# Kernel tuning notes

Measured on AMD Instinct MI355X. Metric: run time of the kernel, lower is better.

## Reference

```python
import jax, jax.numpy as jnp
import numpy as np
from functools import partial

NUM_HEADS = 12
NUM_CLUSTERS = 98
LN_EPS = 1e-5
INF = 1e10


def _ln(x, g, b):
    m = x.mean(-1, keepdims=True)
    v = ((x - m) ** 2).mean(-1, keepdims=True)
    return (x - m) / jnp.sqrt(v + LN_EPS) * g + b


def _agglom(dist, num_clusters):
    # dist: [T,T] precomputed distances; average-linkage agglomerative clustering.
    T = dist.shape[0]
    D = dist.at[jnp.arange(T), jnp.arange(T)].set(INF)
    sizes = jnp.ones((T,), dist.dtype)
    labels = jnp.arange(T)
    active = jnp.ones((T,), bool)

    def step(_, state):
        D, sizes, labels, active = state
        Dm = jnp.where(active[:, None] & active[None, :], D, INF)
        idx = jnp.argmin(Dm)
        i0, j0 = idx // T, idx % T
        i = jnp.minimum(i0, j0)
        j = jnp.maximum(i0, j0)
        ni, nj = sizes[i], sizes[j]
        # Lance-Williams update for average linkage
        newd = (ni * D[i] + nj * D[j]) / (ni + nj)
        D = D.at[i, :].set(newd).at[:, i].set(newd)
        D = D.at[i, i].set(INF)
        D = D.at[j, :].set(INF).at[:, j].set(INF)
        sizes = sizes.at[i].set(ni + nj)
        labels = jnp.where(labels == j, i, labels)
        active = active.at[j].set(False)
        return (D, sizes, labels, active)

    D, sizes, labels, active = jax.lax.fori_loop(0, T - num_clusters, step, (D, sizes, labels, active))
    rank = jnp.cumsum(active.astype(jnp.int32)) - 1  # compact active cluster ids to 0..K-1
    return rank[labels]


def reference(x, attn_size, n1_g, n1_b, w_qkv, w_proj, b_proj, n2_g, n2_b, w_fc1, b_fc1, w_fc2, b_fc2):
    B, N, C = x.shape
    H = NUM_HEADS
    hd = C // H
    # --- Attention_ToMe ---
    h = _ln(x, n1_g, n1_b)
    qkv = (h @ w_qkv).reshape(B, N, 3, H, hd).transpose(2, 0, 3, 1, 4)
    q, k, v = qkv[0], qkv[1], qkv[2]
    metric = k.mean(axis=1)  # [B,N,hd]
    attn = jnp.einsum('bhqd,bhkd->bhqk', q, k) * (hd ** -0.5)
    attn = attn + jnp.log(attn_size)[:, None, None, :, 0]  # size bias (log 1 = 0 first block)
    attn = jax.nn.softmax(attn, axis=-1)
    xa = jnp.einsum('bhqk,bhkd->bqhd', attn, v).reshape(B, N, C)
    x = x + xa @ w_proj + b_proj
    # --- agglomerative clustering (no_grad in original) ---
    m = jax.lax.stop_gradient(metric)
    m = m / jnp.linalg.norm(m, axis=-1, keepdims=True)
    dist = 1.0 - jnp.einsum('bnd,bmd->bnm', m, m)[:, 1:, 1:]  # drop cls token
    labels = jax.vmap(partial(_agglom, num_clusters=NUM_CLUSTERS))(dist)  # [B,N-1]
    labels = jnp.concatenate([jnp.zeros((B, 1), labels.dtype), labels + 1], axis=1)  # cls -> cluster 0
    # --- weighted-average merge (scatter_reduce sum expressed as onehot matmul) ---
    Kt = NUM_CLUSTERS + 1
    onehot = (labels[:, :, None] == jnp.arange(Kt)[None, None, :]).astype(x.dtype)  # [B,N,Kt]
    xs = jnp.einsum('bnk,bnc->bkc', onehot, x * attn_size)
    size_new = jnp.einsum('bnk,bnc->bkc', onehot, attn_size)
    x = xs / size_new
    # --- MLP ---
    h = _ln(x, n2_g, n2_b)
    h = jax.nn.gelu(h @ w_fc1 + b_fc1, approximate=False)
    x = x + h @ w_fc2 + b_fc2
    return x, size_new, labels


def setup_inputs() -> dict:
    key = jax.random.key(0)
    ks = jax.random.split(key, 6)
    B, N, C = 64, 197, 768
    Hf = 4 * C
    s = lambda d: 1.0 / np.sqrt(d)
    return {
        'x': jax.random.normal(ks[0], (B, N, C), jnp.float32),
        'attn_size': jnp.ones((B, N, 1), jnp.float32),
        'n1_g': jnp.ones((C,), jnp.float32),
        'n1_b': jnp.zeros((C,), jnp.float32),
        'w_qkv': jax.random.normal(ks[1], (C, 3 * C), jnp.float32) * s(C),
        'w_proj': jax.random.normal(ks[2], (C, C), jnp.float32) * s(C),
        'b_proj': jnp.zeros((C,), jnp.float32),
        'n2_g': jnp.ones((C,), jnp.float32),
        'n2_b': jnp.zeros((C,), jnp.float32),
        'w_fc1': jax.random.normal(ks[3], (C, Hf), jnp.float32) * s(C),
        'b_fc1': jnp.zeros((Hf,), jnp.float32),
        'w_fc2': jax.random.normal(ks[4], (Hf, C), jnp.float32) * s(Hf),
        'b_fc2': jnp.zeros((C,), jnp.float32),
    }
```

## Files before the change

### kernel.cpp

```cpp
#include <hip/hip_runtime.h>
#include <hip/hip_bf16.h>
#include <math.h>

#define INF_ 1e10f
#define LGKM0() asm volatile("s_waitcnt lgkmcnt(0)" ::: "memory")

static constexpr int B_  = 64;
static constexpr int N_  = 197;
static constexpr int C_  = 768;
static constexpr int H_  = 12;
static constexpr int T_  = 196;
static constexpr int KC_ = 98;
static constexpr int KT_ = 99;
static constexpr int HF_ = 3072;

typedef __attribute__((ext_vector_type(8))) short short8v;
typedef __attribute__((ext_vector_type(4))) float f32x4;
typedef __attribute__((ext_vector_type(4))) int int4v;

__device__ __forceinline__ float wave_sum(float v){
#pragma unroll
  for(int o=32;o;o>>=1) v += __shfl_down(v,o);
  return v;
}

__device__ __forceinline__ ushort f2bf(float v){
  __hip_bfloat16 t = __float2bfloat16(v);
  return *reinterpret_cast<const ushort*>(&t);
}

__device__ __forceinline__ unsigned long long packkey(float v, int r, int a){
  unsigned int bb = __float_as_uint(v);
  bb ^= (bb & 0x80000000u) ? 0xFFFFFFFFu : 0x80000000u;
  return ((unsigned long long)bb<<32) | (unsigned)(r<<8) | (unsigned)a;
}
__device__ __forceinline__ float unpackval(unsigned long long key){
  unsigned u = (unsigned)(key>>32);
  u = (u & 0x80000000u) ? (u ^ 0x80000000u) : ~u;
  return __uint_as_float(u);
}

__global__ __launch_bounds__(256) void ln_kernel(const float* __restrict__ in,
    const float* __restrict__ g, const float* __restrict__ bb,
    float* __restrict__ outf, __hip_bfloat16* __restrict__ outb){
  int row = blockIdx.x;
  const float* xr = in + (size_t)row*C_;
  int tid = threadIdx.x;
  float v0=xr[tid], v1=xr[tid+256], v2=xr[tid+512];
  __shared__ float sred[4];
  __shared__ float smean, svar;
  float s = wave_sum(v0+v1+v2);
  int w=tid>>6, l=tid&63;
  if(l==0) sred[w]=s;
  __syncthreads();
  if(tid==0) smean = (sred[0]+sred[1]+sred[2]+sred[3])/(float)C_;
  __syncthreads();
  float m = smean;
  float d0=v0-m, d1=v1-m, d2=v2-m;
  float q = wave_sum(d0*d0+d1*d1+d2*d2);
  if(l==0) sred[w]=q;
  __syncthreads();
  if(tid==0) svar = (sred[0]+sred[1]+sred[2]+sred[3])/(float)C_;
  __syncthreads();
  float sq = sqrtf(svar + 1e-5f);
  float y0 = d0/sq*g[tid]     + bb[tid];
  float y1 = d1/sq*g[tid+256] + bb[tid+256];
  float y2 = d2/sq*g[tid+512] + bb[tid+512];
  if(outf){
    float* orow = outf + (size_t)row*C_;
    orow[tid]=y0; orow[tid+256]=y1; orow[tid+512]=y2;
  }
  if(outb){
    __hip_bfloat16* orow = outb + (size_t)row*C_;
    orow[tid]=__float2bfloat16(y0); orow[tid+256]=__float2bfloat16(y1); orow[tid+512]=__float2bfloat16(y2);
  }
}

__global__ __launch_bounds__(256) void wmean_kernel(const float* __restrict__ w,
    float* __restrict__ Wm){
  int t = blockIdx.x*256 + threadIdx.x;
  if(t >= C_*64) return;
  int c = t>>6, d = t&63;
  const float* p = w + (size_t)c*(3*C_) + C_ + d;
  float s=0.f;
#pragma unroll
  for(int h=0;h<H_;h++) s += p[h*64];
  Wm[t] = s*(1.0f/12.0f);
}

__global__ __launch_bounds__(256) void transpose_bf16(const float* __restrict__ w,
    __hip_bfloat16* __restrict__ wt, int K, int N){
  __shared__ float tile[32][33];
  int n0 = blockIdx.x*32, k0 = blockIdx.y*32;
  int tx = threadIdx.x&31, ty = threadIdx.x>>5;
  for(int r=ty;r<32;r+=8) tile[r][tx] = w[(size_t)(k0+r)*N + n0+tx];
  __syncthreads();
  for(int r=ty;r<32;r+=8) wt[(size_t)(n0+r)*K + k0+tx] = __float2bfloat16(tile[tx][r]);
}

template<int EPI>
__global__ __launch_bounds__(256) void gemm_bf16(const ushort* __restrict__ A,
    const ushort* __restrict__ Bt, const float* __restrict__ bias,
    const float* __restrict__ res, void* __restrict__ Cout,
    int M, int N, int K){
  constexpr int BM=128, BN=128, BK=32;
  __shared__ ushort As[BM][40];
  __shared__ ushort Bs[BN][40];
  int tid = threadIdx.x;
  int bm = blockIdx.y*BM, bn = blockIdx.x*BN;
  int w = tid>>6, l = tid&63;
  int wm = (w>>1)*64, wn = (w&1)*64;
  int lr = l&15, lc = l>>4;
  f32x4 acc[4][4] = {};
  for(int k0=0;k0<K;k0+=BK){
#pragma unroll
    for(int s=0;s<2;s++){
      int cid = tid + s*256;
      int r = cid>>2, ch = cid&3;
      int4v va = {0,0,0,0};
      if(bm+r < M) va = *reinterpret_cast<const int4v*>(A + (size_t)(bm+r)*K + k0 + ch*8);
      *reinterpret_cast<int4v*>(&As[r][ch*8]) = va;
      int4v vb = *reinterpret_cast<const int4v*>(Bt + (size_t)(bn+r)*K + k0 + ch*8);
      *reinterpret_cast<int4v*>(&Bs[r][ch*8]) = vb;
    }
    __syncthreads();
    short8v af[4], bfr[4];
#pragma unroll
    for(int f=0; f<4; f++){
      af[f]  = *reinterpret_cast<const short8v*>(&As[wm + f*16 + lr][lc*8]);
      bfr[f] = *reinterpret_cast<const short8v*>(&Bs[wn + f*16 + lr][lc*8]);
    }
#pragma unroll
    for(int i=0;i<4;i++)
#pragma unroll
      for(int j=0;j<4;j++)
        acc[i][j] = __builtin_amdgcn_mfma_f32_16x16x32_bf16(af[i], bfr[j], acc[i][j], 0,0,0);
    __syncthreads();
  }
#pragma unroll
  for(int i=0;i<4;i++){
    int rbase = bm + wm + i*16 + lc*4;
#pragma unroll
    for(int j=0;j<4;j++){
      int col = bn + wn + j*16 + lr;
#pragma unroll
      for(int r=0;r<4;r++){
        int row = rbase + r;
        if(row >= M) continue;
        size_t idx = (size_t)row*N + col;
        float v = acc[i][j][r];
        if constexpr(EPI==1 || EPI==3) ((float*)Cout)[idx] = (res[idx] + v) + bias[col];
        if constexpr(EPI==2){
          v += bias[col];
          v = 0.5f*v*(1.0f+erff(v*0.70710678118654752f));
          ((__hip_bfloat16*)Cout)[idx] = __float2bfloat16(v);
        }
        if constexpr(EPI==4) ((__hip_bfloat16*)Cout)[idx] = __float2bfloat16(v);
      }
    }
  }
}

__global__ __launch_bounds__(256) void metric_gemm(const float* __restrict__ h,
    const float* __restrict__ Wm, float* __restrict__ mnorm){
  int row0 = blockIdx.x*16;
  __shared__ float hs[16][C_];
  int tid = threadIdx.x;
  int w = tid>>6, l = tid&63;
  for(int t=tid; t<16*C_; t+=256)
    hs[t/C_][t%C_] = h[(size_t)row0*C_ + t];
  __syncthreads();
  float a0=0.f,a1=0.f,a2=0.f,a3=0.f;
#pragma unroll 4
  for(int c=0;c<C_;c++){
    float wv = Wm[c*64+l];
    a0 = fmaf(hs[w*4+0][c], wv, a0);
    a1 = fmaf(hs[w*4+1][c], wv, a1);
    a2 = fmaf(hs[w*4+2][c], wv, a2);
    a3 = fmaf(hs[w*4+3][c], wv, a3);
  }
  float accs[4] = {a0,a1,a2,a3};
#pragma unroll
  for(int r=0;r<4;r++){
    float acc = accs[r];
    float q = acc*acc;
#pragma unroll
    for(int o=32;o;o>>=1) q += __shfl_xor(q,o);
    float nrm = sqrtf(q);
    int row = row0 + w*4 + r;
    int bb = row / N_, n = row - bb*N_;
    if(n>=1) mnorm[((size_t)bb*T_+(n-1))*64+l] = acc/nrm;
  }
}

__global__ __launch_bounds__(256) void attn_mfma(const ushort* __restrict__ qkv,
    const float* __restrict__ attn_size, __hip_bfloat16* __restrict__ xa){
  int h = blockIdx.x, b = blockIdx.y;
  __shared__ ushort Ks[208][72];
  __shared__ ushort VsT[64][232];
  __shared__ ushort Ps[4][16][232];
  __shared__ float lsz[208];
  int tid = threadIdx.x;
  int w = tid>>6, l = tid&63;
  int lr = l&15, lc = l>>4;
  const size_t QROW = 3*C_;
  for(int t=tid; t<208*64; t+=256){
    int n=t>>6, d=t&63;
    ushort v = 0;
    if(n<197) v = qkv[((size_t)(b*N_+n))*QROW + C_ + h*64 + d];
    Ks[n][d] = v;
  }
  for(int t=tid; t<232*64; t+=256){
    int n=t>>6, d=t&63;
    ushort v = 0;
    if(n<197) v = qkv[((size_t)(b*N_+n))*QROW + 2*C_ + h*64 + d];
    VsT[d][n] = v;
  }
  for(int t=tid;t<208;t+=256) lsz[t] = (t<197)? logf(attn_size[b*N_+t]) : 0.f;
  for(int c=l; c<16*24; c+=64){ int rr=c/24, cc=208+(c%24); Ps[w][rr][cc]=0; }
  __syncthreads();

  for(int qt=w; qt<13; qt+=4){
    int qrow = min(qt*16 + lr, 196);
    const ushort* qp = qkv + ((size_t)(b*N_+qrow))*QROW + h*64;
    short8v aq0 = *reinterpret_cast<const short8v*>(qp + lc*8);
    short8v aq1 = *reinterpret_cast<const short8v*>(qp + 32 + lc*8);
    float sc[13][4];
#pragma unroll
    for(int t=0;t<13;t++){
      short8v b0 = *reinterpret_cast<const short8v*>(&Ks[t*16+lr][lc*8]);
      short8v b1 = *reinterpret_cast<const short8v*>(&Ks[t*16+lr][32+lc*8]);
      f32x4 a = {0.f,0.f,0.f,0.f};
      a = __builtin_amdgcn_mfma_f32_16x16x32_bf16(aq0, b0, a, 0,0,0);
      a = __builtin_amdgcn_mfma_f32_16x16x32_bf16(aq1, b1, a, 0,0,0);
      float ls = lsz[t*16+lr];
      bool mask = (t==12) && (lr>=5);
#pragma unroll
      for(int r=0;r<4;r++) sc[t][r] = mask ? -1e30f : (a[r]*0.125f + ls);
    }
    float rsum[4];
#pragma unroll
    for(int r=0;r<4;r++){
      float m=-1e30f;
#pragma unroll
      for(int t=0;t<13;t++) m = fmaxf(m, sc[t][r]);
#pragma unroll
      for(int o=1;o<16;o<<=1) m = fmaxf(m, __shfl_xor(m,o));
      float s=0.f;
#pragma unroll
      for(int t=0;t<13;t++){ float p=expf(sc[t][r]-m); sc[t][r]=p; s+=p; }
#pragma unroll
      for(int o=1;o<16;o<<=1) s += __shfl_xor(s,o);
      rsum[r]=s;
    }
#pragma unroll
    for(int t=0;t<13;t++)
#pragma unroll
      for(int r=0;r<4;r++)
        Ps[w][lc*4+r][t*16+lr] = f2bf(sc[t][r]);
    LGKM0();
    short8v ap[7];
#pragma unroll
    for(int ks=0;ks<7;ks++) ap[ks] = *reinterpret_cast<const short8v*>(&Ps[w][lr][ks*32 + lc*8]);
#pragma unroll
    for(int f=0; f<4; f++){
      f32x4 o = {0.f,0.f,0.f,0.f};
#pragma unroll
      for(int ks=0;ks<7;ks++){
        short8v bv = *reinterpret_cast<const short8v*>(&VsT[f*16+lr][ks*32 + lc*8]);
        o = __builtin_amdgcn_mfma_f32_16x16x32_bf16(ap[ks], bv, o, 0,0,0);
      }
#pragma unroll
      for(int r=0;r<4;r++){
        int q = qt*16 + lc*4 + r;
        if(q<197) xa[((size_t)(b*N_+q))*C_ + h*64 + f*16 + lr] = __float2bfloat16(o[r]/rsum[r]);
      }
    }
  }
}

__global__ __launch_bounds__(256) void cluster_kernel(const float* __restrict__ mnorm,
    int* __restrict__ labs_ws, float* __restrict__ labs_out){
  int b = blockIdx.x;
  __shared__ unsigned long long rowkey[T_];
  __shared__ unsigned long long gkey[2][4];
  __shared__ unsigned long long scratch[4];
  __shared__ float D[T_][T_+1];
  __shared__ float sizes[T_];
  __shared__ int   labels[T_];
  __shared__ int   active[T_];
  __shared__ int   rlist[T_];
  __shared__ int   rcnt;
  int tid = threadIdx.x;
  int w = tid>>6, l = tid&63;
  const float* mb = mnorm + (size_t)b*T_*64;

  for(int t=tid;t<T_*T_;t+=256){
    int r=t/T_, c=t%T_;
    float dot=0.0f;
    for(int d=0;d<64;d++) dot += mb[r*64+d]*mb[c*64+d];
    D[r][c] = (r==c) ? INF_ : (1.0f - dot);
  }
  for(int t=tid;t<T_;t+=256){ sizes[t]=1.0f; labels[t]=t; active[t]=1; }
  if(tid<8) gkey[tid>>2][tid&3] = ~0ULL;
  __syncthreads();
  if(tid<T_){
    float bvv=INF_; int ba=0;
    for(int c=0;c<T_;c++){ float v=D[tid][c]; if(v<bvv){ bvv=v; ba=c; } }
    rowkey[tid] = packkey(bvv, tid, ba);
  }
  __syncthreads();

  for(int it=0; it<T_-KC_; it++){
    int p = it&1;
    unsigned long long key = (tid<T_) ? rowkey[tid] : ~0ULL;
    atomicMin(&gkey[p][w], key);
    if(tid==0) rcnt = 0;
    __syncthreads();
    unsigned long long g0=gkey[p][0], g1=gkey[p][1];
    unsigned long long g2=gkey[p][2], g3=gkey[p][3];
    unsigned long long ga = g0<g1?g0:g1, gb2 = g2<g3?g2:g3;
    unsigned long long g  = ga<gb2?ga:gb2;
    int i = (int)((g>>8)&0xFF);
    int j = (int)(g&0xFF);
    float ni = sizes[i], nj = sizes[j];
    int k=tid;
    if(k<T_){
      float di=D[i][k], dj=D[j][k];
      unsigned long long oldkey = rowkey[k];
      float oldrm = unpackval(oldkey);
      int oldarg = (int)(oldkey & 0xFF);
      bool kact = (k!=i) && (k!=j) && (active[k]!=0);
      float nd = kact ? (ni*di + nj*dj) / (ni+nj) : INF_;
      D[i][k]=nd; D[k][i]=nd; D[j][k]=INF_; D[k][j]=INF_;
      if(labels[k]==j) labels[k]=i;
      if(k==i){
        int q=atomicAdd(&rcnt,1); rlist[q]=k;
      } else if(k==j){
        rowkey[k] = packkey(INF_, k, 0);
      } else if(kact){
        if(oldarg==i){
          if(nd<=oldrm) rowkey[k] = packkey(nd, k, i);
          else { int q=atomicAdd(&rcnt,1); rlist[q]=k; }
        } else if(oldarg==j){
          if(nd<=oldrm) rowkey[k] = packkey(nd, k, i);
          else { int q=atomicAdd(&rcnt,1); rlist[q]=k; }
        } else {
          if(nd<oldrm || (nd==oldrm && i<oldarg)) rowkey[k] = packkey(nd, k, i);
        }
      }
    }
    if(tid==0){ sizes[i]=ni+nj; active[j]=0; }
    if(l==0) atomicExch(&gkey[p^1][w], ~0ULL);
    __syncthreads();
    int nr = rcnt;
    for(int q=w; q<nr; q+=4){
      int rr = rlist[q];
      if(l==0) atomicExch(&scratch[w], ~0ULL);
      unsigned long long lk = ~0ULL;
      for(int cc=l; cc<T_; cc+=64){
        unsigned long long ck = packkey(D[rr][cc], rr, cc);
        if(ck<lk) lk=ck;
      }
      atomicMin(&scratch[w], lk);
      LGKM0();
      unsigned long long rk = scratch[w];
      if(l==0) rowkey[rr] = rk;
    }
    __syncthreads();
  }

  if(tid==0){
    int c=0;
    for(int t=0;t<T_;t++){ c += active[t]; rlist[t]=c-1; }
    labs_ws[b*N_]=0; labs_out[b*N_]=0.0f;
  }
  __syncthreads();
  for(int t=tid;t<T_;t+=256){
    int lab = rlist[labels[t]] + 1;
    labs_ws[b*N_+1+t] = lab;
    labs_out[b*N_+1+t] = (float)lab;
  }
}

__global__ __launch_bounds__(256) void merge_kernel(const float* __restrict__ x1,
    const float* __restrict__ asz, const int* __restrict__ labs,
    float* __restrict__ x2, float* __restrict__ size_out){
  int chunk = blockIdx.x;
  int b = blockIdx.y;
  __shared__ float acc[KT_][256];
  __shared__ int   lab[N_];
  __shared__ float sz[N_];
  __shared__ float ssum[KT_];
  int tid = threadIdx.x;
  for(int t=tid;t<N_;t+=256){ lab[t]=labs[b*N_+t]; sz[t]=asz[b*N_+t]; }
#pragma unroll
  for(int k=0;k<KT_;k++) acc[k][tid]=0.f;
  __syncthreads();
  if(tid<KT_){
    float s=0.f;
    for(int n=0;n<N_;n++) if(lab[n]==tid) s += sz[n];
    ssum[tid]=s;
  }
  int c = chunk*256 + tid;
  const float* xb = x1 + (size_t)b*N_*C_ + c;
  for(int n=0;n<N_;n++){
    float v = xb[(size_t)n*C_];
    int k = lab[n];
    acc[k][tid] += v * sz[n];
  }
  __syncthreads();
  for(int k=0;k<KT_;k++)
    x2[((size_t)(b*KT_+k))*C_ + c] = acc[k][tid] / ssum[k];
  if(chunk==0 && tid<KT_) size_out[b*KT_+tid] = ssum[tid];
}

extern "C" void kernel_launch(void* const* d_in, const int* in_sizes, int n_in,
                              void* d_out, int out_size, void* d_ws, size_t ws_size,
                              hipStream_t stream){
  const float* x      = (const float*)d_in[0];
  const float* asz    = (const float*)d_in[1];
  const float* n1_g   = (const float*)d_in[2];
  const float* n1_b   = (const float*)d_in[3];
  const float* w_qkv  = (const float*)d_in[4];
  const float* w_proj = (const float*)d_in[5];
  const float* b_proj = (const float*)d_in[6];
  const float* n2_g   = (const float*)d_in[7];
  const float* n2_b   = (const float*)d_in[8];
  const float* w_fc1  = (const float*)d_in[9];
  const float* b_fc1  = (const float*)d_in[10];
  const float* w_fc2  = (const float*)d_in[11];
  const float* b_fc2  = (const float*)d_in[12];

  const size_t ROWS = (size_t)B_*N_;
  const size_t M2   = (size_t)B_*KT_;
  float* ws = (float*)d_ws;

  float* h     = ws;
  float* qkvR  = h + ROWS*C_;
  __hip_bfloat16* qkvb = (__hip_bfloat16*)qkvR;
  float* x2    = qkvR;
  __hip_bfloat16* h2b = (__hip_bfloat16*)(qkvR + M2*C_);
  __hip_bfloat16* h3b = (__hip_bfloat16*)(qkvR + M2*C_ + M2*C_/2);
  __hip_bfloat16* hb  = (__hip_bfloat16*)(qkvR + ROWS*3*C_);
  __hip_bfloat16* xa  = hb;
  float* mnorm = (float*)(hb) + ROWS*C_/2;
  float* Wm    = mnorm + (size_t)B_*T_*64;
  __hip_bfloat16* wqkvT = (__hip_bfloat16*)(Wm + C_*64);
  __hip_bfloat16* wprojT= (__hip_bfloat16*)((float*)wqkvT + (size_t)3*C_*C_/2);
  __hip_bfloat16* wfc1T = (__hip_bfloat16*)((float*)wprojT + (size_t)C_*C_/2);
  __hip_bfloat16* wfc2T = (__hip_bfloat16*)((float*)wfc1T + (size_t)C_*HF_/2);
  int*   labs  = (int*)((float*)wfc2T + (size_t)HF_*C_/2);
  float* x1    = h;

  float* out     = (float*)d_out;
  float* out_sz  = out + M2*C_;
  float* out_lab = out_sz + M2;

  ln_kernel<<<dim3((unsigned)ROWS),256,0,stream>>>(x, n1_g, n1_b, h, hb);
  wmean_kernel<<<dim3(192),256,0,stream>>>(w_qkv, Wm);
  transpose_bf16<<<dim3(72,24),256,0,stream>>>(w_qkv, wqkvT, C_, 3*C_);
  transpose_bf16<<<dim3(24,24),256,0,stream>>>(w_proj, wprojT, C_, C_);
  transpose_bf16<<<dim3(96,24),256,0,stream>>>(w_fc1, wfc1T, C_, HF_);
  transpose_bf16<<<dim3(24,96),256,0,stream>>>(w_fc2, wfc2T, HF_, C_);

  gemm_bf16<4><<<dim3(18,99),256,0,stream>>>((const ushort*)hb, (const ushort*)wqkvT,
      nullptr, nullptr, qkvb, (int)ROWS, 3*C_, C_);
  metric_gemm<<<dim3(788),256,0,stream>>>(h, Wm, mnorm);
  attn_mfma<<<dim3(H_,B_),256,0,stream>>>((const ushort*)qkvb, asz, xa);
  gemm_bf16<1><<<dim3(6,99),256,0,stream>>>((const ushort*)xa, (const ushort*)wprojT,
      b_proj, x, x1, (int)ROWS, C_, C_);

  cluster_kernel<<<dim3(B_),256,0,stream>>>(mnorm, labs, out_lab);
  merge_kernel<<<dim3(3,B_),256,0,stream>>>(x1, asz, labs, x2, out_sz);

  ln_kernel<<<dim3((unsigned)M2),256,0,stream>>>(x2, n2_g, n2_b, nullptr, h2b);
  gemm_bf16<2><<<dim3(24,50),256,0,stream>>>((const ushort*)h2b, (const ushort*)wfc1T,
      b_fc1, nullptr, h3b, (int)M2, HF_, C_);
  gemm_bf16<3><<<dim3(6,50),256,0,stream>>>((const ushort*)h3b, (const ushort*)wfc2T,
      b_fc2, x2, out, (int)M2, C_, HF_);
}
```

Baseline: 1.158 ms.

## Cut clustering loop to one barrier per merge with register state and triple-buffered keys

Restructures the agglomerative clustering loop so each merge step needs a single __syncthreads instead of two. Per-row min keys, sizes, labels and active flags move into registers. The merged row's new min is found by an atomicMin reduction folded into the update. Global-min keys are triple-buffered so resetting the slot for a later step does not race with readers, and dirty rows are rescanned serially by their owning thread instead of cooperatively by a wave. The barrier saving is traded for possible thread divergence on the serial 196-element rescans.

```diff
diff --git a/kernel.cpp b/kernel.cpp
--- a/kernel.cpp
+++ b/kernel.cpp
@@ -282,17 +282,15 @@
 __global__ __launch_bounds__(256) void cluster_kernel(const float* __restrict__ mnorm,
     int* __restrict__ labs_ws, float* __restrict__ labs_out){
   int b = blockIdx.x;
-  __shared__ unsigned long long rowkey[T_];
-  __shared__ unsigned long long gkey[2][4];
-  __shared__ unsigned long long scratch[4];
   __shared__ float D[T_][T_+1];
-  __shared__ float sizes[T_];
-  __shared__ int   labels[T_];
-  __shared__ int   active[T_];
-  __shared__ int   rlist[T_];
-  __shared__ int   rcnt;
-  int tid = threadIdx.x;
-  int w = tid>>6, l = tid&63;
+  __shared__ unsigned long long gkey[3][4];
+  __shared__ unsigned long long rikey[3][4];
+  __shared__ float szl[2][256];
+  __shared__ int labels_s[T_];
+  __shared__ int act_s[T_];
+  __shared__ int rank_s[T_];
+  int tid = threadIdx.x;
+  int w = tid>>6;
   const float* mb = mnorm + (size_t)b*T_*64;
 
   for(int t=tid;t<T_*T_;t+=256){
@@ -301,83 +299,88 @@
     for(int d=0;d<64;d++) dot += mb[r*64+d]*mb[c*64+d];
     D[r][c] = (r==c) ? INF_ : (1.0f - dot);
   }
-  for(int t=tid;t<T_;t+=256){ sizes[t]=1.0f; labels[t]=t; active[t]=1; }
-  if(tid<8) gkey[tid>>2][tid&3] = ~0ULL;
-  __syncthreads();
+  if(tid<12) gkey[tid>>2][tid&3] = ~0ULL;
+  else if(tid<24) rikey[(tid-12)>>2][(tid-12)&3] = ~0ULL;
+  szl[0][tid]=1.0f; szl[1][tid]=1.0f;
+  __syncthreads();
+
+  unsigned long long mykey = ~0ULL;
+  float szk = 1.0f;
+  int labk = tid;
+  int actk = (tid<T_) ? 1 : 0;
   if(tid<T_){
-    float bvv=INF_; int ba=0;
-    for(int c=0;c<T_;c++){ float v=D[tid][c]; if(v<bvv){ bvv=v; ba=c; } }
-    rowkey[tid] = packkey(bvv, tid, ba);
-  }
-  __syncthreads();
-
+    float bv=INF_; int ba=0;
+    for(int c=0;c<T_;c++){ float v=D[tid][c]; if(v<bv){bv=v;ba=c;} }
+    mykey = packkey(bv, tid, ba);
+    atomicMin(&gkey[0][w], mykey);
+  }
+  __syncthreads();
+
+  int iprev = -1;
   for(int it=0; it<T_-KC_; it++){
-    int p = it&1;
-    unsigned long long key = (tid<T_) ? rowkey[tid] : ~0ULL;
-    atomicMin(&gkey[p][w], key);
-    if(tid==0) rcnt = 0;
-    __syncthreads();
-    unsigned long long g0=gkey[p][0], g1=gkey[p][1];
-    unsigned long long g2=gkey[p][2], g3=gkey[p][3];
-    unsigned long long ga = g0<g1?g0:g1, gb2 = g2<g3?g2:g3;
-    unsigned long long g  = ga<gb2?ga:gb2;
+    int A = it%3, Bs = (it+1)%3, Cs = (it+2)%3;
+    int pA = it&1, pB = pA^1;
+    unsigned long long g=~0ULL, rik=~0ULL;
+#pragma unroll
+    for(int s=0;s<4;s++){ unsigned long long v=gkey[A][s]; if(v<g) g=v; }
+#pragma unroll
+    for(int s=0;s<4;s++){ unsigned long long v=rikey[A][s]; if(v<rik) rik=v; }
+    if(tid==iprev) mykey = rik;
+    if(rik<g) g = rik;
     int i = (int)((g>>8)&0xFF);
     int j = (int)(g&0xFF);
-    float ni = sizes[i], nj = sizes[j];
-    int k=tid;
-    if(k<T_){
+    float ni = szl[pA][i], nj = szl[pA][j];
+    if(tid==i) szk = ni+nj;
+    if(tid==j) actk = 0;
+    if(labk==j) labk = i;
+    szl[pB][tid] = szk;
+    if((tid&63)==0){ gkey[Cs][w]=~0ULL; rikey[Cs][w]=~0ULL; }
+    if(tid<T_){
+      int k = tid;
       float di=D[i][k], dj=D[j][k];
-      unsigned long long oldkey = rowkey[k];
-      float oldrm = unpackval(oldkey);
-      int oldarg = (int)(oldkey & 0xFF);
-      bool kact = (k!=i) && (k!=j) && (active[k]!=0);
-      float nd = kact ? (ni*di + nj*dj) / (ni+nj) : INF_;
+      float oldrm = unpackval(mykey);
+      int oldarg = (int)(mykey & 0xFF);
+      bool kact = (k!=i) && (k!=j) && (actk!=0);
+      float nd = kact ? (ni*di + nj*dj)/(ni+nj) : INF_;
       D[i][k]=nd; D[k][i]=nd; D[j][k]=INF_; D[k][j]=INF_;
-      if(labels[k]==j) labels[k]=i;
+      atomicMin(&rikey[Bs][w], packkey(nd, i, k));
       if(k==i){
-        int q=atomicAdd(&rcnt,1); rlist[q]=k;
       } else if(k==j){
-        rowkey[k] = packkey(INF_, k, 0);
+        mykey = packkey(INF_, k, 0);
       } else if(kact){
+        bool dirty=false;
         if(oldarg==i){
-          if(nd<=oldrm) rowkey[k] = packkey(nd, k, i);
-          else { int q=atomicAdd(&rcnt,1); rlist[q]=k; }
+          if(nd<=oldrm) mykey=packkey(nd,k,i); else dirty=true;
         } else if(oldarg==j){
-          if(nd<=oldrm) rowkey[k] = packkey(nd, k, i);
-          else { int q=atomicAdd(&rcnt,1); rlist[q]=k; }
+          if(nd<=oldrm) mykey=packkey(nd,k,i); else dirty=true;
         } else {
-          if(nd<oldrm || (nd==oldrm && i<oldarg)) rowkey[k] = packkey(nd, k, i);
+          if(nd<oldrm || (nd==oldrm && i<oldarg)) mykey=packkey(nd,k,i);
         }
+        if(dirty){
+          float v=INF_; int cb=0;
+          for(int cc=0;cc<T_;cc++){
+            float vv = D[k][cc];
+            if(vv<v){ v=vv; cb=cc; }
+          }
+          mykey = packkey(v,k,cb);
+        }
+        atomicMin(&gkey[Bs][w], mykey);
       }
     }
-    if(tid==0){ sizes[i]=ni+nj; active[j]=0; }
-    if(l==0) atomicExch(&gkey[p^1][w], ~0ULL);
+    iprev = i;
     __syncthreads();
-    int nr = rcnt;
-    for(int q=w; q<nr; q+=4){
-      int rr = rlist[q];
-      if(l==0) atomicExch(&scratch[w], ~0ULL);
-      unsigned long long lk = ~0ULL;
-      for(int cc=l; cc<T_; cc+=64){
-        unsigned long long ck = packkey(D[rr][cc], rr, cc);
-        if(ck<lk) lk=ck;
-      }
-      atomicMin(&scratch[w], lk);
-      LGKM0();
-      unsigned long long rk = scratch[w];
-      if(l==0) rowkey[rr] = rk;
-    }
-    __syncthreads();
-  }
-
+  }
+
+  if(tid<T_){ labels_s[tid]=labk; act_s[tid]=actk; }
+  __syncthreads();
   if(tid==0){
     int c=0;
-    for(int t=0;t<T_;t++){ c += active[t]; rlist[t]=c-1; }
+    for(int t=0;t<T_;t++){ c += act_s[t]; rank_s[t]=c-1; }
     labs_ws[b*N_]=0; labs_out[b*N_]=0.0f;
   }
   __syncthreads();
   for(int t=tid;t<T_;t+=256){
-    int lab = rlist[labels[t]] + 1;
+    int lab = rank_s[labels_s[t]] + 1;
     labs_ws[b*N_+1+t] = lab;
     labs_out[b*N_+1+t] = (float)lab;
   }
```

Result: slower. 1.498 ms (+29.4%).

## Run clustering concurrently with attention in one launch and merge weight-prep kernels

Applied to the files above, without the earlier changes.

Merges the weight-mean and four weight-transpose kernels into a single prep kernel that dispatches on block index. Fuses the serial per-batch clustering kernel with the attention kernel into one launch, with the first 64 blocks doing clustering and the rest doing attention over a shared-memory union. The aim is to hide the long, low-occupancy clustering loop behind the attention work and to cut launch overhead. The union is sized by the larger clustering layout, so attention blocks now reserve more LDS, which may lower their occupancy.

```diff
diff --git a/kernel.cpp b/kernel.cpp
--- a/kernel.cpp
+++ b/kernel.cpp
@@ -76,23 +76,33 @@
   }
 }
 
-__global__ __launch_bounds__(256) void wmean_kernel(const float* __restrict__ w,
-    float* __restrict__ Wm){
-  int t = blockIdx.x*256 + threadIdx.x;
-  if(t >= C_*64) return;
-  int c = t>>6, d = t&63;
-  const float* p = w + (size_t)c*(3*C_) + C_ + d;
-  float s=0.f;
-#pragma unroll
-  for(int h=0;h<H_;h++) s += p[h*64];
-  Wm[t] = s*(1.0f/12.0f);
-}
-
-__global__ __launch_bounds__(256) void transpose_bf16(const float* __restrict__ w,
-    __hip_bfloat16* __restrict__ wt, int K, int N){
+__global__ __launch_bounds__(256) void prep_kernel(const float* __restrict__ w_qkv,
+    const float* __restrict__ w_proj, const float* __restrict__ w_fc1,
+    const float* __restrict__ w_fc2, float* __restrict__ Wm,
+    __hip_bfloat16* __restrict__ wqkvT, __hip_bfloat16* __restrict__ wprojT,
+    __hip_bfloat16* __restrict__ wfc1T, __hip_bfloat16* __restrict__ wfc2T){
+  int bid = blockIdx.x;
+  int tid = threadIdx.x;
+  if(bid < 192){
+    int t = bid*256 + tid;
+    if(t >= C_*64) return;
+    int c = t>>6, d = t&63;
+    const float* p = w_qkv + (size_t)c*(3*C_) + C_ + d;
+    float s=0.f;
+#pragma unroll
+    for(int h=0;h<H_;h++) s += p[h*64];
+    Wm[t] = s*(1.0f/12.0f);
+    return;
+  }
+  bid -= 192;
+  const float* w; __hip_bfloat16* wt; int K, N, nbx;
+  if(bid < 1728){ w=w_qkv; wt=wqkvT; K=C_; N=3*C_; nbx=72; }
+  else if(bid < 1728+576){ bid-=1728; w=w_proj; wt=wprojT; K=C_; N=C_; nbx=24; }
+  else if(bid < 1728+576+2304){ bid-=1728+576; w=w_fc1; wt=wfc1T; K=C_; N=HF_; nbx=96; }
+  else { bid-=1728+576+2304; w=w_fc2; wt=wfc2T; K=HF_; N=C_; nbx=24; }
   __shared__ float tile[32][33];
-  int n0 = blockIdx.x*32, k0 = blockIdx.y*32;
-  int tx = threadIdx.x&31, ty = threadIdx.x>>5;
+  int n0 = (bid%nbx)*32, k0 = (bid/nbx)*32;
+  int tx = tid&31, ty = tid>>5;
   for(int r=ty;r<32;r+=8) tile[r][tx] = w[(size_t)(k0+r)*N + n0+tx];
   __syncthreads();
   for(int r=ty;r<32;r+=8) wt[(size_t)(n0+r)*K + k0+tx] = __float2bfloat16(tile[tx][r]);
@@ -193,13 +203,121 @@
   }
 }
 
-__global__ __launch_bounds__(256) void attn_mfma(const ushort* __restrict__ qkv,
-    const float* __restrict__ attn_size, __hip_bfloat16* __restrict__ xa){
-  int h = blockIdx.x, b = blockIdx.y;
-  __shared__ ushort Ks[208][72];
-  __shared__ ushort VsT[64][232];
-  __shared__ ushort Ps[4][16][232];
-  __shared__ float lsz[208];
+struct ClusterSh {
+  float D[T_][T_+1];
+  unsigned long long rowkey[T_];
+  unsigned long long gkey[2][4];
+  unsigned long long scratch[4];
+  float sizes[T_];
+  int labels[T_];
+  int active[T_];
+  int rlist[T_];
+  int rcnt;
+};
+struct AttnSh {
+  ushort Ks[208][72];
+  ushort VsT[64][232];
+  ushort Ps[4][16][232];
+  float lsz[208];
+};
+union FusedSh { ClusterSh c; AttnSh a; };
+
+__device__ void cluster_body(ClusterSh& S, const float* __restrict__ mnorm,
+    int* __restrict__ labs_ws, float* __restrict__ labs_out, int b){
+  int tid = threadIdx.x;
+  int w = tid>>6, l = tid&63;
+  const float* mb = mnorm + (size_t)b*T_*64;
+
+  for(int t=tid;t<T_*T_;t+=256){
+    int r=t/T_, c=t%T_;
+    float dot=0.0f;
+    for(int d=0;d<64;d++) dot += mb[r*64+d]*mb[c*64+d];
+    S.D[r][c] = (r==c) ? INF_ : (1.0f - dot);
+  }
+  for(int t=tid;t<T_;t+=256){ S.sizes[t]=1.0f; S.labels[t]=t; S.active[t]=1; }
+  if(tid<8) S.gkey[tid>>2][tid&3] = ~0ULL;
+  __syncthreads();
+  if(tid<T_){
+    float bvv=INF_; int ba=0;
+    for(int c=0;c<T_;c++){ float v=S.D[tid][c]; if(v<bvv){ bvv=v; ba=c; } }
+    S.rowkey[tid] = packkey(bvv, tid, ba);
+  }
+  __syncthreads();
+
+  for(int it=0; it<T_-KC_; it++){
+    int p = it&1;
+    unsigned long long key = (tid<T_) ? S.rowkey[tid] : ~0ULL;
+    atomicMin(&S.gkey[p][w], key);
+    if(tid==0) S.rcnt = 0;
+    __syncthreads();
+    unsigned long long g0=S.gkey[p][0], g1=S.gkey[p][1];
+    unsigned long long g2=S.gkey[p][2], g3=S.gkey[p][3];
+    unsigned long long ga = g0<g1?g0:g1, gb2 = g2<g3?g2:g3;
+    unsigned long long g  = ga<gb2?ga:gb2;
+    int i = (int)((g>>8)&0xFF);
+    int j = (int)(g&0xFF);
+    float ni = S.sizes[i], nj = S.sizes[j];
+    int k=tid;
+    if(k<T_){
+      float di=S.D[i][k], dj=S.D[j][k];
+      unsigned long long oldkey = S.rowkey[k];
+      float oldrm = unpackval(oldkey);
+      int oldarg = (int)(oldkey & 0xFF);
+      bool kact = (k!=i) && (k!=j) && (S.active[k]!=0);
+      float nd = kact ? (ni*di + nj*dj) / (ni+nj) : INF_;
+      S.D[i][k]=nd; S.D[k][i]=nd; S.D[j][k]=INF_; S.D[k][j]=INF_;
+      if(S.labels[k]==j) S.labels[k]=i;
+      if(k==i){
+        int q=atomicAdd(&S.rcnt,1); S.rlist[q]=k;
+      } else if(k==j){
+        S.rowkey[k] = packkey(INF_, k, 0);
+      } else if(kact){
+        if(oldarg==i){
+          if(nd<=oldrm) S.rowkey[k] = packkey(nd, k, i);
+          else { int q=atomicAdd(&S.rcnt,1); S.rlist[q]=k; }
+        } else if(oldarg==j){
+          if(nd<=oldrm) S.rowkey[k] = packkey(nd, k, i);
+          else { int q=atomicAdd(&S.rcnt,1); S.rlist[q]=k; }
+        } else {
+          if(nd<oldrm || (nd==oldrm && i<oldarg)) S.rowkey[k] = packkey(nd, k, i);
+        }
+      }
+    }
+    if(tid==0){ S.sizes[i]=ni+nj; S.active[j]=0; }
+    if(l==0) atomicExch(&S.gkey[p^1][w], ~0ULL);
+    __syncthreads();
+    int nr = S.rcnt;
+    for(int q=w; q<nr; q+=4){
+      int rr = S.rlist[q];
+      if(l==0) atomicExch(&S.scratch[w], ~0ULL);
+      unsigned long long lk = ~0ULL;
+      for(int cc=l; cc<T_; cc+=64){
+        unsigned long long ck = packkey(S.D[rr][cc], rr, cc);
+        if(ck<lk) lk=ck;
+      }
+      atomicMin(&S.scratch[w], lk);
+      LGKM0();
+      unsigned long long rk = S.scratch[w];
+      if(l==0) S.rowkey[rr] = rk;
+    }
+    __syncthreads();
+  }
+
+  if(tid==0){
+    int c=0;
+    for(int t=0;t<T_;t++){ c += S.active[t]; S.rlist[t]=c-1; }
+    labs_ws[b*N_]=0; labs_out[b*N_]=0.0f;
+  }
+  __syncthreads();
+  for(int t=tid;t<T_;t+=256){
+    int lab = S.rlist[S.labels[t]] + 1;
+    labs_ws[b*N_+1+t] = lab;
+    labs_out[b*N_+1+t] = (float)lab;
+  }
+}
+
+__device__ void attn_body(AttnSh& S, const ushort* __restrict__ qkv,
+    const float* __restrict__ attn_size, __hip_bfloat16* __restrict__ xa, int h, int b){
   int tid = threadIdx.x;
   int w = tid>>6, l = tid&63;
   int lr = l&15, lc = l>>4;
@@ -208,16 +326,16 @@
     int n=t>>6, d=t&63;
     ushort v = 0;
     if(n<197) v = qkv[((size_t)(b*N_+n))*QROW + C_ + h*64 + d];
-    Ks[n][d] = v;
+    S.Ks[n][d] = v;
   }
   for(int t=tid; t<232*64; t+=256){
     int n=t>>6, d=t&63;
     ushort v = 0;
     if(n<197) v = qkv[((size_t)(b*N_+n))*QROW + 2*C_ + h*64 + d];
-    VsT[d][n] = v;
-  }
-  for(int t=tid;t<208;t+=256) lsz[t] = (t<197)? logf(attn_size[b*N_+t]) : 0.f;
-  for(int c=l; c<16*24; c+=64){ int rr=c/24, cc=208+(c%24); Ps[w][rr][cc]=0; }
+    S.VsT[d][n] = v;
+  }
+  for(int t=tid;t<208;t+=256) S.lsz[t] = (t<197)? logf(attn_size[b*N_+t]) : 0.f;
+  for(int c=l; c<16*24; c+=64){ int rr=c/24, cc=208+(c%24); S.Ps[w][rr][cc]=0; }
   __syncthreads();
 
   for(int qt=w; qt<13; qt+=4){
@@ -228,12 +346,12 @@
     float sc[13][4];
 #pragma unroll
     for(int t=0;t<13;t++){
-      short8v b0 = *reinterpret_cast<const short8v*>(&Ks[t*16+lr][lc*8]);
-      short8v b1 = *reinterpret_cast<const short8v*>(&Ks[t*16+lr][32+lc*8]);
+      short8v b0 = *reinterpret_cast<const short8v*>(&S.Ks[t*16+lr][lc*8]);
+      short8v b1 = *reinterpret_cast<const short8v*>(&S.Ks[t*16+lr][32+lc*8]);
       f32x4 a = {0.f,0.f,0.f,0.f};
       a = __builtin_amdgcn_mfma_f32_16x16x32_bf16(aq0, b0, a, 0,0,0);
       a = __builtin_amdgcn_mfma_f32_16x16x32_bf16(aq1, b1, a, 0,0,0);
-      float ls = lsz[t*16+lr];
+      float ls = S.lsz[t*16+lr];
       bool mask = (t==12) && (lr>=5);
 #pragma unroll
       for(int r=0;r<4;r++) sc[t][r] = mask ? -1e30f : (a[r]*0.125f + ls);
@@ -257,17 +375,17 @@
     for(int t=0;t<13;t++)
 #pragma unroll
       for(int r=0;r<4;r++)
-        Ps[w][lc*4+r][t*16+lr] = f2bf(sc[t][r]);
+        S.Ps[w][lc*4+r][t*16+lr] = f2bf(sc[t][r]);
     LGKM0();
     short8v ap[7];
 #pragma unroll
-    for(int ks=0;ks<7;ks++) ap[ks] = *reinterpret_cast<const short8v*>(&Ps[w][lr][ks*32 + lc*8]);
+    for(int ks=0;ks<7;ks++) ap[ks] = *reinterpret_cast<const short8v*>(&S.Ps[w][lr][ks*32 + lc*8]);
 #pragma unroll
     for(int f=0; f<4; f++){
       f32x4 o = {0.f,0.f,0.f,0.f};
 #pragma unroll
       for(int ks=0;ks<7;ks++){
-        short8v bv = *reinterpret_cast<const short8v*>(&VsT[f*16+lr][ks*32 + lc*8]);
+        short8v bv = *reinterpret_cast<const short8v*>(&S.VsT[f*16+lr][ks*32 + lc*8]);
         o = __builtin_amdgcn_mfma_f32_16x16x32_bf16(ap[ks], bv, o, 0,0,0);
       }
 #pragma unroll
@@ -279,107 +397,17 @@
   }
 }
 
-__global__ __launch_bounds__(256) void cluster_kernel(const float* __restrict__ mnorm,
-    int* __restrict__ labs_ws, float* __restrict__ labs_out){
-  int b = blockIdx.x;
-  __shared__ unsigned long long rowkey[T_];
-  __shared__ unsigned long long gkey[2][4];
-  __shared__ unsigned long long scratch[4];
-  __shared__ float D[T_][T_+1];
-  __shared__ float sizes[T_];
-  __shared__ int   labels[T_];
-  __shared__ int   active[T_];
-  __shared__ int   rlist[T_];
-  __shared__ int   rcnt;
-  int tid = threadIdx.x;
-  int w = tid>>6, l = tid&63;
-  const float* mb = mnorm + (size_t)b*T_*64;
-
-  for(int t=tid;t<T_*T_;t+=256){
-    int r=t/T_, c=t%T_;
-    float dot=0.0f;
-    for(int d=0;d<64;d++) dot += mb[r*64+d]*mb[c*64+d];
-    D[r][c] = (r==c) ? INF_ : (1.0f - dot);
-  }
-  for(int t=tid;t<T_;t+=256){ sizes[t]=1.0f; labels[t]=t; active[t]=1; }
-  if(tid<8) gkey[tid>>2][tid&3] = ~0ULL;
-  __syncthreads();
-  if(tid<T_){
-    float bvv=INF_; int ba=0;
-    for(int c=0;c<T_;c++){ float v=D[tid][c]; if(v<bvv){ bvv=v; ba=c; } }
-    rowkey[tid] = packkey(bvv, tid, ba);
-  }
-  __syncthreads();
-
-  for(int it=0; it<T_-KC_; it++){
-    int p = it&1;
-    unsigned long long key = (tid<T_) ? rowkey[tid] : ~0ULL;
-    atomicMin(&gkey[p][w], key);
-    if(tid==0) rcnt = 0;
-    __syncthreads();
-    unsigned long long g0=gkey[p][0], g1=gkey[p][1];
-    unsigned long long g2=gkey[p][2], g3=gkey[p][3];
-    unsigned long long ga = g0<g1?g0:g1, gb2 = g2<g3?g2:g3;
-    unsigned long long g  = ga<gb2?ga:gb2;
-    int i = (int)((g>>8)&0xFF);
-    int j = (int)(g&0xFF);
-    float ni = sizes[i], nj = sizes[j];
-    int k=tid;
-    if(k<T_){
-      float di=D[i][k], dj=D[j][k];
-      unsigned long long oldkey = rowkey[k];
-      float oldrm = unpackval(oldkey);
-      int oldarg = (int)(oldkey & 0xFF);
-      bool kact = (k!=i) && (k!=j) && (active[k]!=0);
-      float nd = kact ? (ni*di + nj*dj) / (ni+nj) : INF_;
-      D[i][k]=nd; D[k][i]=nd; D[j][k]=INF_; D[k][j]=INF_;
-      if(labels[k]==j) labels[k]=i;
-      if(k==i){
-        int q=atomicAdd(&rcnt,1); rlist[q]=k;
-      } else if(k==j){
-        rowkey[k] = packkey(INF_, k, 0);
-      } else if(kact){
-        if(oldarg==i){
-          if(nd<=oldrm) rowkey[k] = packkey(nd, k, i);
-          else { int q=atomicAdd(&rcnt,1); rlist[q]=k; }
-        } else if(oldarg==j){
-          if(nd<=oldrm) rowkey[k] = packkey(nd, k, i);
-          else { int q=atomicAdd(&rcnt,1); rlist[q]=k; }
-        } else {
-          if(nd<oldrm || (nd==oldrm && i<oldarg)) rowkey[k] = packkey(nd, k, i);
-        }
-      }
-    }
-    if(tid==0){ sizes[i]=ni+nj; active[j]=0; }
-    if(l==0) atomicExch(&gkey[p^1][w], ~0ULL);
-    __syncthreads();
-    int nr = rcnt;
-    for(int q=w; q<nr; q+=4){
-      int rr = rlist[q];
-      if(l==0) atomicExch(&scratch[w], ~0ULL);
-      unsigned long long lk = ~0ULL;
-      for(int cc=l; cc<T_; cc+=64){
-        unsigned long long ck = packkey(D[rr][cc], rr, cc);
-        if(ck<lk) lk=ck;
-      }
-      atomicMin(&scratch[w], lk);
-      LGKM0();
-      unsigned long long rk = scratch[w];
-      if(l==0) rowkey[rr] = rk;
-    }
-    __syncthreads();
-  }
-
-  if(tid==0){
-    int c=0;
-    for(int t=0;t<T_;t++){ c += active[t]; rlist[t]=c-1; }
-    labs_ws[b*N_]=0; labs_out[b*N_]=0.0f;
-  }
-  __syncthreads();
-  for(int t=tid;t<T_;t+=256){
-    int lab = rlist[labels[t]] + 1;
-    labs_ws[b*N_+1+t] = lab;
-    labs_out[b*N_+1+t] = (float)lab;
+__global__ __launch_bounds__(256) void cluster_attn_fused(
+    const float* __restrict__ mnorm, int* __restrict__ labs_ws, float* __restrict__ labs_out,
+    const ushort* __restrict__ qkv, const float* __restrict__ attn_size,
+    __hip_bfloat16* __restrict__ xa){
+  __shared__ FusedSh sh;
+  int bid = blockIdx.x;
+  if(bid < B_){
+    cluster_body(sh.c, mnorm, labs_ws, labs_out, bid);
+  } else {
+    int idx = bid - B_;
+    attn_body(sh.a, qkv, attn_size, xa, idx % H_, idx / H_);
   }
 }
 
@@ -458,20 +486,18 @@
   float* out_lab = out_sz + M2;
 
   ln_kernel<<<dim3((unsigned)ROWS),256,0,stream>>>(x, n1_g, n1_b, h, hb);
-  wmean_kernel<<<dim3(192),256,0,stream>>>(w_qkv, Wm);
-  transpose_bf16<<<dim3(72,24),256,0,stream>>>(w_qkv, wqkvT, C_, 3*C_);
-  transpose_bf16<<<dim3(24,24),256,0,stream>>>(w_proj, wprojT, C_, C_);
-  transpose_bf16<<<dim3(96,24),256,0,stream>>>(w_fc1, wfc1T, C_, HF_);
-  transpose_bf16<<<dim3(24,96),256,0,stream>>>(w_fc2, wfc2T, HF_, C_);
+  prep_kernel<<<dim3(192 + 1728 + 576 + 2304 + 2304),256,0,stream>>>(
+      w_qkv, w_proj, w_fc1, w_fc2, Wm, wqkvT, wprojT, wfc1T, wfc2T);
 
   gemm_bf16<4><<<dim3(18,99),256,0,stream>>>((const ushort*)hb, (const ushort*)wqkvT,
       nullptr, nullptr, qkvb, (int)ROWS, 3*C_, C_);
   metric_gemm<<<dim3(788),256,0,stream>>>(h, Wm, mnorm);
-  attn_mfma<<<dim3(H_,B_),256,0,stream>>>((const ushort*)qkvb, asz, xa);
+
+  cluster_attn_fused<<<dim3(B_ + H_*B_),256,0,stream>>>(mnorm, labs, out_lab,
+      (const ushort*)qkvb, asz, xa);
+
   gemm_bf16<1><<<dim3(6,99),256,0,stream>>>((const ushort*)xa, (const ushort*)wprojT,
       b_proj, x, x1, (int)ROWS, C_, C_);
-
-  cluster_kernel<<<dim3(B_),256,0,stream>>>(mnorm, labs, out_lab);
   merge_kernel<<<dim3(3,B_),256,0,stream>>>(x1, asz, labs, x2, out_sz);
 
   ln_kernel<<<dim3((unsigned)M2),256,0,stream>>>(x2, n2_g, n2_b, nullptr, h2b);
```

New measurement: 994.5 us. -14.1%, faster.
